# Kernel optimization log

Measured on AMD Instinct MI355X. Metric: run time of the kernel, lower is better.

## Reference

```python
import jax, jax.numpy as jnp
import numpy as np

K = 3          # kernel size (3x3 branch of SConv_2d)
STRIDE = 1
PAD = 1
NONCENTER = jnp.array([0, 1, 2, 3, 5, 6, 7, 8])      # drop center (idx 4) before sort
REORDER = jnp.array([0, 1, 2, 3, 8, 4, 5, 6, 7])     # reinsert center in the middle


def setup_inputs() -> dict:
    key = jax.random.key(0)
    k1, k2, k3, k4 = jax.random.split(key, 4)
    B, Cin, H, Wd = 8, 64, 128, 128
    Cout = 128
    x = jax.random.normal(k1, (B, Cin, H, Wd), dtype=jnp.float32)
    Coefficient = jax.random.normal(k2, (K * K, K * K), dtype=jnp.float32)
    W = jax.random.normal(k3, (Cout, Cin, K, K), dtype=jnp.float32) * 0.05
    b = jax.random.normal(k4, (Cout,), dtype=jnp.float32) * 0.05
    return {"x": x, "Coefficient": Coefficient, "W": W, "b": b}


def reference(x, Coefficient, W, b):
    # pad (same=False -> constant padding PAD on all sides)
    xp = jnp.pad(x, ((0, 0), (0, 0), (PAD, PAD), (PAD, PAD)))
    B, C, Hp, Wp = xp.shape
    Ho = (Hp - K) // STRIDE + 1
    Wo = (Wp - K) // STRIDE + 1
    # unfold: patches[b, kh*K+kw, c, h, w] == torch unfold+view+permute layout [B, KH*KW, C, H*W]
    patches = jnp.stack(
        [xp[:, :, i:i + Ho * STRIDE:STRIDE, j:j + Wo * STRIDE:STRIDE]
         for i in range(K) for j in range(K)], axis=1)           # [B, 9, C, Ho, Wo]
    center = patches[:, 4:5]                                      # [B, 1, C, Ho, Wo]
    y = jnp.einsum('bjchw,ij->bichw', patches, Coefficient)       # [B, 9, C, Ho, Wo]
    ys = jnp.sort(y[:, NONCENTER], axis=1)                        # sort 8 non-center taps
    z = jnp.concatenate([ys, center], axis=1)                     # [B, 9, C, Ho, Wo]
    z = z[:, REORDER]
    # view(B, KH, KW, C, H, W).permute(0,3,4,1,5,2) -> [B, C, KH*H, KW*W]
    z = z.reshape(B, K, K, C, Ho, Wo).transpose(0, 3, 4, 1, 5, 2).reshape(B, C, K * Ho, K * Wo)
    out = jax.lax.conv_general_dilated(
        z, W, window_strides=(K, K), padding='VALID',
        dimension_numbers=('NCHW', 'OIHW', 'NCHW'))
    return out + b[None, :, None, None]
```

## Files before the change

### kernel.cpp

```cpp
#include <hip/hip_runtime.h>
#include <hip/hip_bf16.h>


#define B_   8
#define C_   64
#define H_   128
#define W_   128
#define CO_  128
#define K_   576
#define MT   32
#define SROW 584
#define TB   4

typedef __attribute__((ext_vector_type(8)))  short  short8;
typedef __attribute__((ext_vector_type(8)))  __bf16 bf16x8;
typedef __attribute__((ext_vector_type(16))) float  f32x16;
typedef __attribute__((ext_vector_type(2)))  float  f32x2;

__device__ __forceinline__ void cswap2(f32x2 &a, f32x2 &b) {
    f32x2 lo = __builtin_elementwise_min(a, b);
    f32x2 hi = __builtin_elementwise_max(a, b);
    a = lo; b = hi;
}

__device__ __forceinline__ ushort f2bf(float f) {
    union { float f; unsigned u; } v; v.f = f;
    unsigned r = v.u + 0x7fffu + ((v.u >> 16) & 1u);
    return (ushort)(r >> 16);
}

__device__ __forceinline__ unsigned pack2bf(float lo, float hi) {
    union { __hip_bfloat162 h; unsigned u; } cv;
    cv.h = __float22bfloat162_rn(make_float2(lo, hi));
    return cv.u;
}

__global__ __launch_bounds__(256) void conv_W_bf16(const float* __restrict__ Wg,
                                                   ushort* __restrict__ Wb) {
    int i = blockIdx.x * 256 + threadIdx.x;
    if (i >= CO_ * K_) return;
    const int e    = i & 7;
    const int lane = (i >> 3) & 63;
    const int t9   = i >> 9;
    const int nt   = t9 / 36;
    const int ks   = t9 - nt * 36;
    const int co   = nt * 32 + (lane & 31);
    const int kp   = ks * 16 + (lane >> 5) * 8 + e;
    int c, t;
    if (kp < 512) { const int rc = kp >> 3; t = kp & 7; c = ((rc & 7) << 3) | (rc >> 3); }
    else          { c = kp - 512; t = 8; }
    Wb[i] = f2bf(Wg[co * K_ + c * 9 + t]);
}

__device__ __forceinline__ void load_row(const float* __restrict__ xb, int hy,
                                         int w, bool wint, float out[4]) {
    if (wint && (unsigned)hy < (unsigned)H_) {
        float4 v; __builtin_memcpy(&v, xb + hy * W_ + (w - 1), 16);
        out[0] = v.x; out[1] = v.y; out[2] = v.z; out[3] = v.w;
    } else {
        const bool hok = (unsigned)hy < (unsigned)H_;
        const int hc = min(max(hy, 0), H_ - 1);
        const int wm = w - 1;
        const int wc = min(max(wm, 0), W_ - 4);
        const int s  = wm - wc;
        float4 v; __builtin_memcpy(&v, xb + hc * W_ + wc, 16);
        const float r0 = (s < 0) ? 0.f : ((s > 0) ? v.y : v.x);
        const float r1 = (s < 0) ? v.x : ((s > 0) ? v.z : v.y);
        const float r2 = (s < 0) ? v.y : ((s > 0) ? v.w : v.z);
        const float r3 = (s < 0) ? v.z : ((s > 0) ? 0.f : v.w);
        out[0] = hok ? r0 : 0.f; out[1] = hok ? r1 : 0.f;
        out[2] = hok ? r2 : 0.f; out[3] = hok ? r3 : 0.f;
    }
}

__device__ __forceinline__ void zstore_tile(const float (&rr)[4][4],
                                            const float* __restrict__ Coef,
                                            char* bufb, int rcb, int tailb, int pw) {
    #pragma unroll
    for (int hl = 0; hl < 2; ++hl) {
        f32x2 p2[9];
        #pragma unroll
        for (int dy = 0; dy < 3; ++dy)
            #pragma unroll
            for (int dx = 0; dx < 3; ++dx)
                p2[dy * 3 + dx] = (f32x2){ rr[hl + dy][dx], rr[hl + dy][dx + 1] };

        f32x2 v2[8];
        #pragma unroll
        for (int ii = 0; ii < 8; ++ii) {
            const int i = ii + (ii >> 2);
            f32x2 acc = p2[0] * Coef[i * 9];
            #pragma unroll
            for (int jj = 1; jj < 9; ++jj) acc += p2[jj] * Coef[i * 9 + jj];
            v2[ii] = acc;
        }

        cswap2(v2[0],v2[1]); cswap2(v2[2],v2[3]); cswap2(v2[4],v2[5]); cswap2(v2[6],v2[7]);
        cswap2(v2[0],v2[2]); cswap2(v2[1],v2[3]); cswap2(v2[4],v2[6]); cswap2(v2[5],v2[7]);
        cswap2(v2[1],v2[2]); cswap2(v2[5],v2[6]);
        cswap2(v2[0],v2[4]); cswap2(v2[1],v2[5]); cswap2(v2[2],v2[6]); cswap2(v2[3],v2[7]);
        cswap2(v2[2],v2[4]); cswap2(v2[3],v2[5]);
        cswap2(v2[1],v2[2]); cswap2(v2[3],v2[4]); cswap2(v2[5],v2[6]);

        f32x2 z2[9] = { v2[0], v2[1], v2[2], v2[3], p2[4],
                        v2[4], v2[5], v2[6], v2[7] };

        char* zb0 = bufb + (size_t)(hl * 16 + pw * 2) * (SROW * 2);
        char* zb1 = zb0 + SROW * 2;
        uint4 q0 = make_uint4(pack2bf(z2[0][0], z2[1][0]), pack2bf(z2[2][0], z2[3][0]),
                              pack2bf(z2[4][0], z2[5][0]), pack2bf(z2[6][0], z2[7][0]));
        uint4 q1 = make_uint4(pack2bf(z2[0][1], z2[1][1]), pack2bf(z2[2][1], z2[3][1]),
                              pack2bf(z2[4][1], z2[5][1]), pack2bf(z2[6][1], z2[7][1]));
        *(uint4*)(zb0 + rcb) = q0;
        *(uint4*)(zb1 + rcb) = q1;
        *(ushort*)(zb0 + tailb) = f2bf(z2[8][0]);
        *(ushort*)(zb1 + tailb) = f2bf(z2[8][1]);
    }
}

__global__ __launch_bounds__(512, 4) void sconv_mfma(
    const float* __restrict__ x,
    const float* __restrict__ Coef,
    const ushort* __restrict__ Wb,
    const float* __restrict__ bias,
    float* __restrict__ out)
{
    __shared__ __align__(16) ushort Zl[2][MT * SROW];

    const int tid = threadIdx.x;
    const int bx  = blockIdx.x;
    const int wq  = bx & 7;
    const int hq  = (bx >> 3) & 15;
    const int b   = bx >> 7;
    const int w0  = wq * 16;
    const int h0b = hq * 8;

    const int wave = tid >> 6;
    const int lane = tid & 63;
    const int nt   = wave & 3;
    const int r31  = lane & 31;
    const int u    = lane >> 5;
    const ushort* bptr = Wb + ((size_t)(nt * 36) * 64 + lane) * 8;

    const int j  = (tid >> 3) & 7;
    const int c  = wave + 8 * j;
    const int pw = tid & 7;
    const int w  = w0 + pw * 2;
    const float* xb = x + ((size_t)(b * C_ + c)) * (H_ * W_);
    const bool wint = (w0 >= 16) && (w0 <= 96);
    const int rcb   = (wave * 8 + j) << 4;
    const int tailb = 1024 + 2 * c;

    short8 bq[4];
    if (wave < 4) {
        #pragma unroll
        for (int i = 0; i < 4; ++i) bq[i] = *(const short8*)(bptr + i * 512);
    }

    float rr[4][4];
    load_row(xb, h0b - 1, w, wint, rr[0]);
    load_row(xb, h0b + 0, w, wint, rr[1]);
    load_row(xb, h0b + 1, w, wint, rr[2]);
    load_row(xb, h0b + 2, w, wint, rr[3]);
    zstore_tile(rr, Coef, (char*)&Zl[0][0], rcb, tailb, pw);
    __syncthreads();

    for (int t = 0; t < TB; ++t) {
        if (t < TB - 1) {
            #pragma unroll
            for (int q2 = 0; q2 < 4; ++q2) { rr[0][q2] = rr[2][q2]; rr[1][q2] = rr[3][q2]; }
            const int h0n = h0b + 2 * (t + 1);
            load_row(xb, h0n + 1, w, wint, rr[2]);
            load_row(xb, h0n + 2, w, wint, rr[3]);
            zstore_tile(rr, Coef, (char*)&Zl[(t + 1) & 1][0], rcb, tailb, pw);
        }
        if (wave < 4) {
            const char* abase = (const char*)&Zl[t & 1][0] + (size_t)r31 * (SROW * 2) + u * 16;
            bf16x8 aq[2];
            aq[0] = *(const bf16x8*)(abase + 0);
            aq[1] = *(const bf16x8*)(abase + 32);
            f32x16 acc = {};
            #pragma unroll
            for (int ks = 0; ks < 36; ++ks) {
                bf16x8 a  = aq[ks & 1];
                short8 bb = bq[ks & 3];
                if (ks + 2 < 36)
                    aq[ks & 1] = *(const bf16x8*)(abase + (ks + 2) * 32);
                if (ks + 4 < 36)
                    bq[ks & 3] = *(const short8*)(bptr + (ks + 4) * 512);
                acc = __builtin_amdgcn_mfma_f32_32x32x16_bf16(a, __builtin_bit_cast(bf16x8, bb), acc, 0, 0, 0);
            }
            if (t < TB - 1) {
                #pragma unroll
                for (int i = 0; i < 4; ++i) bq[i] = *(const short8*)(bptr + i * 512);
            }
            const int h0t = h0b + 2 * t;
            const int co  = nt * 32 + r31;
            const float bv = bias[co];
            float* obase = out + (((size_t)(b * CO_ + co)) * H_ + h0t) * W_ + w0;
            #pragma unroll
            for (int qq = 0; qq < 4; ++qq) {
                const int roff = qq * 8 + u * 4;
                const int hl   = roff >> 4;
                const int wl   = roff & 15;
                *(float4*)(obase + hl * W_ + wl) =
                    make_float4(acc[qq*4+0] + bv, acc[qq*4+1] + bv,
                                acc[qq*4+2] + bv, acc[qq*4+3] + bv);
            }
        }
        __syncthreads();
    }
}

#define WT 16
__device__ __forceinline__ void cswap(float &a, float &b) {
    float lo = fminf(a, b);
    float hi = fmaxf(a, b);
    a = lo; b = hi;
}
__global__ __launch_bounds__(256) void sconv_fp32(
    const float* __restrict__ x, const float* __restrict__ Coef,
    const float* __restrict__ Wg, const float* __restrict__ bias,
    float* __restrict__ out)
{
    __shared__ float Cf[81];
    __shared__ float Zl[C_ * 9 * WT];
    const int tid = threadIdx.x;
    const int bx  = blockIdx.x;
    const int wt  = bx & 7;
    const int h   = (bx >> 3) & 127;
    const int b   = bx >> 10;
    const int w0  = wt * WT;
    if (tid < 81) Cf[tid] = Coef[tid];
    __syncthreads();
    for (int task = tid; task < C_ * WT; task += 256) {
        const int c = task >> 4, wl = task & 15, w = w0 + wl;
        const float* xb = x + (b * C_ + c) * H_ * W_;
        float p[9];
        #pragma unroll
        for (int dy = 0; dy < 3; ++dy) {
            const int hy = h + dy - 1; const bool hin = (unsigned)hy < (unsigned)H_;
            #pragma unroll
            for (int dx = 0; dx < 3; ++dx) {
                const int wx = w + dx - 1; const bool win = (unsigned)wx < (unsigned)W_;
                p[dy * 3 + dx] = (hin && win) ? xb[hy * W_ + wx] : 0.0f;
            }
        }
        float v[8];
        #pragma unroll
        for (int ii = 0; ii < 8; ++ii) {
            const int i = ii + (ii >> 2);
            float acc = 0.0f;
            #pragma unroll
            for (int jj = 0; jj < 9; ++jj) acc = fmaf(Cf[i * 9 + jj], p[jj], acc);
            v[ii] = acc;
        }
        cswap(v[0], v[1]); cswap(v[2], v[3]); cswap(v[4], v[5]); cswap(v[6], v[7]);
        cswap(v[0], v[2]); cswap(v[1], v[3]); cswap(v[4], v[6]); cswap(v[5], v[7]);
        cswap(v[1], v[2]); cswap(v[5], v[6]);
        cswap(v[0], v[4]); cswap(v[1], v[5]); cswap(v[2], v[6]); cswap(v[3], v[7]);
        cswap(v[2], v[4]); cswap(v[3], v[5]);
        cswap(v[1], v[2]); cswap(v[3], v[4]); cswap(v[5], v[6]);
        const int base = c * 9 * WT + wl;
        Zl[base + 0*WT]=v[0]; Zl[base + 1*WT]=v[1]; Zl[base + 2*WT]=v[2]; Zl[base + 3*WT]=v[3];
        Zl[base + 4*WT]=p[4];
        Zl[base + 5*WT]=v[4]; Zl[base + 6*WT]=v[5]; Zl[base + 7*WT]=v[6]; Zl[base + 8*WT]=v[7];
    }
    __syncthreads();
    const int co = tid >> 1, w0l = (tid & 1) * 8;
    float acc[8];
    #pragma unroll
    for (int i = 0; i < 8; ++i) acc[i] = 0.0f;
    for (int c = 0; c < C_; ++c) {
        #pragma unroll
        for (int t = 0; t < 9; ++t) {
            const float wv = Wg[(co * C_ + c) * 9 + t];
            const float* zp = &Zl[(c * 9 + t) * WT + w0l];
            const float4 za = *(const float4*)zp;
            const float4 zb = *(const float4*)(zp + 4);
            acc[0]=fmaf(za.x,wv,acc[0]); acc[1]=fmaf(za.y,wv,acc[1]);
            acc[2]=fmaf(za.z,wv,acc[2]); acc[3]=fmaf(za.w,wv,acc[3]);
            acc[4]=fmaf(zb.x,wv,acc[4]); acc[5]=fmaf(zb.y,wv,acc[5]);
            acc[6]=fmaf(zb.z,wv,acc[6]); acc[7]=fmaf(zb.w,wv,acc[7]);
        }
    }
    const float bv = bias[co];
    float* op = out + ((b * CO_ + co) * H_ + h) * W_ + w0 + w0l;
    *(float4*)(op)     = make_float4(acc[0]+bv, acc[1]+bv, acc[2]+bv, acc[3]+bv);
    *(float4*)(op + 4) = make_float4(acc[4]+bv, acc[5]+bv, acc[6]+bv, acc[7]+bv);
}

extern "C" void kernel_launch(void* const* d_in, const int* in_sizes, int n_in,
                              void* d_out, int out_size, void* d_ws, size_t ws_size,
                              hipStream_t stream) {
    const float* x    = (const float*)d_in[0];
    const float* Coef = (const float*)d_in[1];
    const float* Wg   = (const float*)d_in[2];
    const float* bias = (const float*)d_in[3];
    float* out = (float*)d_out;

    const size_t need = (size_t)CO_ * K_ * sizeof(ushort);
    if (ws_size >= need) {
        ushort* Wb = (ushort*)d_ws;
        conv_W_bf16<<<(CO_ * K_ + 255) / 256, 256, 0, stream>>>(Wg, Wb);
        sconv_mfma<<<B_ * (H_ / 8) * (W_ / 16), 512, 0, stream>>>(x, Coef, Wb, bias, out);
    } else {
        sconv_fp32<<<B_ * H_ * 8, 256, 0, stream>>>(x, Coef, Wg, bias, out);
    }
}
```

Before: 144.8 us.

## Warp-specialize MFMA kernel into producer and consumer waves with taller row tiles

Splits the 512-thread block so that waves 0-3 only run the MFMA GEMM and waves 4-7 only load x, apply the coefficient mix and sort, and write the bf16 tile into shared memory. The two groups hand off through a double buffer, with each producer wave handling two channels. Rows per block go from 8 to 16 (TB 8), which halves the grid and reduces halo reloads. Prefetch depth grows to 4 A fragments and 6 B fragments. The aim is to overlap the sort/transform work with matrix math, at the cost of fewer blocks, more registers per producer thread, and a more fragile barrier pairing between the two roles.

Result: faster. 139.8 us (-3.4%).

```diff
diff --git a/kernel.cpp b/kernel.cpp
--- a/kernel.cpp
+++ b/kernel.cpp
@@ -10,7 +10,7 @@
 #define K_   576
 #define MT   32
 #define SROW 584
-#define TB   4
+#define TB   8
 
 typedef __attribute__((ext_vector_type(8)))  short  short8;
 typedef __attribute__((ext_vector_type(8)))  __bf16 bf16x8;
@@ -130,73 +130,53 @@
     const int tid = threadIdx.x;
     const int bx  = blockIdx.x;
     const int wq  = bx & 7;
-    const int hq  = (bx >> 3) & 15;
-    const int b   = bx >> 7;
+    const int hq  = (bx >> 3) & 7;
+    const int b   = bx >> 6;
     const int w0  = wq * 16;
-    const int h0b = hq * 8;
+    const int h0b = hq * 16;
 
     const int wave = tid >> 6;
     const int lane = tid & 63;
-    const int nt   = wave & 3;
     const int r31  = lane & 31;
     const int u    = lane >> 5;
-    const ushort* bptr = Wb + ((size_t)(nt * 36) * 64 + lane) * 8;
-
-    const int j  = (tid >> 3) & 7;
-    const int c  = wave + 8 * j;
-    const int pw = tid & 7;
-    const int w  = w0 + pw * 2;
-    const float* xb = x + ((size_t)(b * C_ + c)) * (H_ * W_);
-    const bool wint = (w0 >= 16) && (w0 <= 96);
-    const int rcb   = (wave * 8 + j) << 4;
-    const int tailb = 1024 + 2 * c;
-
-    short8 bq[4];
+
     if (wave < 4) {
-        #pragma unroll
-        for (int i = 0; i < 4; ++i) bq[i] = *(const short8*)(bptr + i * 512);
-    }
-
-    float rr[4][4];
-    load_row(xb, h0b - 1, w, wint, rr[0]);
-    load_row(xb, h0b + 0, w, wint, rr[1]);
-    load_row(xb, h0b + 1, w, wint, rr[2]);
-    load_row(xb, h0b + 2, w, wint, rr[3]);
-    zstore_tile(rr, Coef, (char*)&Zl[0][0], rcb, tailb, pw);
-    __syncthreads();
-
-    for (int t = 0; t < TB; ++t) {
-        if (t < TB - 1) {
-            #pragma unroll
-            for (int q2 = 0; q2 < 4; ++q2) { rr[0][q2] = rr[2][q2]; rr[1][q2] = rr[3][q2]; }
-            const int h0n = h0b + 2 * (t + 1);
-            load_row(xb, h0n + 1, w, wint, rr[2]);
-            load_row(xb, h0n + 2, w, wint, rr[3]);
-            zstore_tile(rr, Coef, (char*)&Zl[(t + 1) & 1][0], rcb, tailb, pw);
-        }
-        if (wave < 4) {
-            const char* abase = (const char*)&Zl[t & 1][0] + (size_t)r31 * (SROW * 2) + u * 16;
-            bf16x8 aq[2];
-            aq[0] = *(const bf16x8*)(abase + 0);
-            aq[1] = *(const bf16x8*)(abase + 32);
+        const int nt = wave;
+        const ushort* bptr = Wb + ((size_t)(nt * 36) * 64 + lane) * 8;
+        const int co  = nt * 32 + r31;
+        const float bv = bias[co];
+
+        short8 bq[6];
+        #pragma unroll
+        for (int i = 0; i < 6; ++i) bq[i] = *(const short8*)(bptr + i * 512);
+
+        __syncthreads();
+
+        for (int t = 0; t < TB; ++t) {
+            const char* abase = (const char*)&Zl[t & 1][0]
+                                + (size_t)r31 * (SROW * 2) + u * 16;
+            bf16x8 aq[4];
+            #pragma unroll
+            for (int i = 0; i < 4; ++i)
+                aq[i] = *(const bf16x8*)(abase + i * 32);
+
             f32x16 acc = {};
             #pragma unroll
             for (int ks = 0; ks < 36; ++ks) {
-                bf16x8 a  = aq[ks & 1];
-                short8 bb = bq[ks & 3];
-                if (ks + 2 < 36)
-                    aq[ks & 1] = *(const bf16x8*)(abase + (ks + 2) * 32);
+                bf16x8 a  = aq[ks & 3];
+                short8 bb = bq[ks % 6];
                 if (ks + 4 < 36)
-                    bq[ks & 3] = *(const short8*)(bptr + (ks + 4) * 512);
-                acc = __builtin_amdgcn_mfma_f32_32x32x16_bf16(a, __builtin_bit_cast(bf16x8, bb), acc, 0, 0, 0);
+                    aq[ks & 3] = *(const bf16x8*)(abase + (ks + 4) * 32);
+                if (ks + 6 < 36)
+                    bq[ks % 6] = *(const short8*)(bptr + (ks + 6) * 512);
+                acc = __builtin_amdgcn_mfma_f32_32x32x16_bf16(
+                          a, __builtin_bit_cast(bf16x8, bb), acc, 0, 0, 0);
             }
             if (t < TB - 1) {
                 #pragma unroll
-                for (int i = 0; i < 4; ++i) bq[i] = *(const short8*)(bptr + i * 512);
+                for (int i = 0; i < 6; ++i) bq[i] = *(const short8*)(bptr + i * 512);
             }
             const int h0t = h0b + 2 * t;
-            const int co  = nt * 32 + r31;
-            const float bv = bias[co];
             float* obase = out + (((size_t)(b * CO_ + co)) * H_ + h0t) * W_ + w0;
             #pragma unroll
             for (int qq = 0; qq < 4; ++qq) {
@@ -207,8 +187,48 @@
                     make_float4(acc[qq*4+0] + bv, acc[qq*4+1] + bv,
                                 acc[qq*4+2] + bv, acc[qq*4+3] + bv);
             }
-        }
+            __syncthreads();
+        }
+    } else {
+        const int wp = wave - 4;
+        const int j  = lane >> 3;
+        const int pw = lane & 7;
+        const int c1 = 8 * j + wp;
+        const int c2 = c1 + 4;
+        const int w  = w0 + pw * 2;
+        const float* xb1 = x + ((size_t)(b * C_ + c1)) * (H_ * W_);
+        const float* xb2 = x + ((size_t)(b * C_ + c2)) * (H_ * W_);
+        const bool wint = (w0 >= 16) && (w0 <= 96);
+        const int rcb1   = (8 * wp + j) << 4;
+        const int rcb2   = rcb1 + 512;
+        const int tailb1 = 1024 + 2 * c1;
+        const int tailb2 = 1024 + 2 * c2;
+
+        float r1[4][4], r2[4][4];
+        load_row(xb1, h0b - 1, w, wint, r1[0]); load_row(xb2, h0b - 1, w, wint, r2[0]);
+        load_row(xb1, h0b + 0, w, wint, r1[1]); load_row(xb2, h0b + 0, w, wint, r2[1]);
+        load_row(xb1, h0b + 1, w, wint, r1[2]); load_row(xb2, h0b + 1, w, wint, r2[2]);
+        load_row(xb1, h0b + 2, w, wint, r1[3]); load_row(xb2, h0b + 2, w, wint, r2[3]);
+        zstore_tile(r1, Coef, (char*)&Zl[0][0], rcb1, tailb1, pw);
+        zstore_tile(r2, Coef, (char*)&Zl[0][0], rcb2, tailb2, pw);
         __syncthreads();
+
+        for (int t = 0; t < TB; ++t) {
+            if (t < TB - 1) {
+                #pragma unroll
+                for (int q2 = 0; q2 < 4; ++q2) {
+                    r1[0][q2] = r1[2][q2]; r1[1][q2] = r1[3][q2];
+                    r2[0][q2] = r2[2][q2]; r2[1][q2] = r2[3][q2];
+                }
+                const int h0n = h0b + 2 * (t + 1);
+                load_row(xb1, h0n + 1, w, wint, r1[2]); load_row(xb2, h0n + 1, w, wint, r2[2]);
+                load_row(xb1, h0n + 2, w, wint, r1[3]); load_row(xb2, h0n + 2, w, wint, r2[3]);
+                char* bufb = (char*)&Zl[(t + 1) & 1][0];
+                zstore_tile(r1, Coef, bufb, rcb1, tailb1, pw);
+                zstore_tile(r2, Coef, bufb, rcb2, tailb2, pw);
+            }
+            __syncthreads();
+        }
     }
 }
 
@@ -303,7 +323,7 @@
     if (ws_size >= need) {
         ushort* Wb = (ushort*)d_ws;
         conv_W_bf16<<<(CO_ * K_ + 255) / 256, 256, 0, stream>>>(Wg, Wb);
-        sconv_mfma<<<B_ * (H_ / 8) * (W_ / 16), 512, 0, stream>>>(x, Coef, Wb, bias, out);
+        sconv_mfma<<<B_ * (H_ / 16) * (W_ / 16), 512, 0, stream>>>(x, Coef, Wb, bias, out);
     } else {
         sconv_fp32<<<B_ * H_ * 8, 256, 0, stream>>>(x, Coef, Wg, bias, out);
     }
```
